# Kernel optimization log

Measured on AMD Instinct MI355X. Metric: run time of the kernel, lower is better.

Reference implementation:

```python
import jax, jax.numpy as jnp
import numpy as np

RESOLUTION = 2 ** 8  # 256
N_POINTS = 2 ** 21


def setup_inputs() -> dict:
    key = jax.random.key(0)
    k1, k2 = jax.random.split(key)
    inp = jax.random.uniform(k1, (N_POINTS, 3), dtype=jnp.float32)
    grid = jax.random.normal(k2, (RESOLUTION, RESOLUTION, RESOLUTION, 3), dtype=jnp.float32) * 0.01
    return {"input": inp, "feature_params": grid}


def reference(input, feature_params):
    R = feature_params.shape[0]
    scaled = input * (R - 1)
    lower = jnp.clip(jnp.floor(scaled).astype(jnp.int32), 0, R - 2)
    upper = jnp.clip(lower + 1, 0, R - 1)
    t = scaled - lower.astype(scaled.dtype)
    xl, yl, zl = lower[:, 0], lower[:, 1], lower[:, 2]
    xu, yu, zu = upper[:, 0], upper[:, 1], upper[:, 2]
    tx, ty, tz = t[:, 0:1], t[:, 1:2], t[:, 2:3]  # (N,1) for broadcast over channels
    # note original indexes grid as [z, y, x]
    c000 = feature_params[zl, yl, xl]
    c001 = feature_params[zl, yl, xu]
    c010 = feature_params[zl, yu, xl]
    c011 = feature_params[zl, yu, xu]
    c100 = feature_params[zu, yl, xl]
    c101 = feature_params[zu, yl, xu]
    c110 = feature_params[zu, yu, xl]
    c111 = feature_params[zu, yu, xu]
    c00 = c000 * (1 - tx) + c001 * tx
    c01 = c010 * (1 - tx) + c011 * tx
    c10 = c100 * (1 - tx) + c101 * tx
    c11 = c110 * (1 - tx) + c111 * tx
    c0 = c00 * (1 - ty) + c01 * ty
    c1 = c10 * (1 - ty) + c11 * ty
    return c0 * (1 - tz) + c1 * tz
```

## Files before the change

### kernel.cpp

```cpp
#include <hip/hip_runtime.h>


#define NB     8192
#define CAP    512u
#define GBLK   1024
#define LAYERF4 1728
#define LAYERF  6912
#define GRIDF4  12582912

#define CUR_OFF   67108864u
#define NEEDED    (67108864u + 32768u)

typedef float f4v __attribute__((ext_vector_type(4)));
typedef float f2v __attribute__((ext_vector_type(2)));
typedef f4v f4u __attribute__((aligned(8)));
typedef f2v f2u __attribute__((aligned(8)));

__device__ __forceinline__ void cell_of(float p, int& l, float& t) {
    float s = p * 255.0f;
    int v = (int)floorf(s);
    v = v < 0 ? 0 : (v > 254 ? 254 : v);
    l = v;
    t = s - (float)v;
}

__device__ __forceinline__ int fine_bin3(float px, float py, float pz) {
    int xl, yl, zl; float tx, ty, tz;
    cell_of(px, xl, tx);
    cell_of(py, yl, ty);
    cell_of(pz, zl, tz);
    return (zl << 5) | (yl >> 3);
}

__device__ __forceinline__ void direct_lerp(const float* __restrict__ grid,
                                            float* __restrict__ out, int i,
                                            int xl, int yl, int zl,
                                            float tx, float ty, float tz) {
    int b00 = (zl * 65536 + yl * 256 + xl) * 3;
    int b01 = b00 + 768, b10 = b00 + 196608, b11 = b10 + 768;
    float s00[6], s01[6], s10[6], s11[6];
#pragma unroll
    for (int k = 0; k < 6; ++k) s00[k] = grid[b00 + k];
#pragma unroll
    for (int k = 0; k < 6; ++k) s01[k] = grid[b01 + k];
#pragma unroll
    for (int k = 0; k < 6; ++k) s10[k] = grid[b10 + k];
#pragma unroll
    for (int k = 0; k < 6; ++k) s11[k] = grid[b11 + k];
#pragma unroll
    for (int c = 0; c < 3; ++c) {
        float c00 = s00[c] * (1.0f - tx) + s00[c + 3] * tx;
        float c01 = s01[c] * (1.0f - tx) + s01[c + 3] * tx;
        float c10 = s10[c] * (1.0f - tx) + s10[c + 3] * tx;
        float c11 = s11[c] * (1.0f - tx) + s11[c + 3] * tx;
        float c0 = c00 * (1.0f - ty) + c01 * ty;
        float c1 = c10 * (1.0f - ty) + c11 * ty;
        out[3 * i + c] = c0 * (1.0f - tz) + c1 * tz;
    }
}

__global__ __launch_bounds__(1024) void k_init(unsigned* __restrict__ cur) {
    int i = blockIdx.x * 1024 + threadIdx.x;
    if (i < NB) cur[i] = (unsigned)i * CAP;
}

__global__ __launch_bounds__(1024) void k_scatter(const float* __restrict__ inp,
                                                  const float* __restrict__ grid,
                                                  float4* __restrict__ binned,
                                                  unsigned* __restrict__ cur,
                                                  float* __restrict__ out, int n) {
    __shared__ unsigned cnt[NB];
    __shared__ unsigned base[NB];
    int t = threadIdx.x;
    int P = n >> 1;
    int stride = gridDim.x * 1024;
    int iters = (P + stride - 1) / stride;

    if ((n & 1) && blockIdx.x == 0 && t == 0) {
        int i = n - 1;
        float px = inp[3 * i], py = inp[3 * i + 1], pz = inp[3 * i + 2];
        int b = fine_bin3(px, py, pz);
        unsigned r = atomicAdd(&cur[b], 1u);
        if (r - (unsigned)b * CAP < CAP) {
            float4 v; v.x = px; v.y = py; v.z = pz; v.w = __uint_as_float((unsigned)i);
            binned[r] = v;
        } else {
            int xl, yl, zl; float tx, ty, tz;
            cell_of(px, xl, tx); cell_of(py, yl, ty); cell_of(pz, zl, tz);
            direct_lerp(grid, out, i, xl, yl, zl, tx, ty, tz);
        }
    }

    for (int it = 0; it < iters; ++it) {
        int pr = it * stride + blockIdx.x * 1024 + t;
        for (int k = t; k < NB; k += 1024) cnt[k] = 0;
        __syncthreads();
        int b0 = 0, b1 = 0; unsigned r0 = 0, r1 = 0;
        float4 p0, p1;
        bool valid = (pr < P);
        if (valid) {
            f4v a = *(const f4u*)(inp + 6 * pr);
            f2v b = *(const f2u*)(inp + 6 * pr + 4);
            p0.x = a.x; p0.y = a.y; p0.z = a.z;
            p0.w = __uint_as_float((unsigned)(2 * pr));
            p1.x = a.w; p1.y = b.x; p1.z = b.y;
            p1.w = __uint_as_float((unsigned)(2 * pr + 1));
            b0 = fine_bin3(p0.x, p0.y, p0.z);
            b1 = fine_bin3(p1.x, p1.y, p1.z);
            r0 = atomicAdd(&cnt[b0], 1u);
            r1 = atomicAdd(&cnt[b1], 1u);
        }
        __syncthreads();
        for (int k = t; k < NB; k += 1024)
            if (cnt[k]) base[k] = atomicAdd(&cur[k], cnt[k]);
        __syncthreads();
        if (valid) {
            unsigned s0 = base[b0] + r0;
            unsigned s1 = base[b1] + r1;
            if (s0 - (unsigned)b0 * CAP < CAP) binned[s0] = p0;
            else {
                int xl, yl, zl; float tx, ty, tz;
                cell_of(p0.x, xl, tx); cell_of(p0.y, yl, ty); cell_of(p0.z, zl, tz);
                direct_lerp(grid, out, 2 * pr, xl, yl, zl, tx, ty, tz);
            }
            if (s1 - (unsigned)b1 * CAP < CAP) binned[s1] = p1;
            else {
                int xl, yl, zl; float tx, ty, tz;
                cell_of(p1.x, xl, tx); cell_of(p1.y, yl, ty); cell_of(p1.z, zl, tz);
                direct_lerp(grid, out, 2 * pr + 1, xl, yl, zl, tx, ty, tz);
            }
        }
        __syncthreads();
    }
}

#define STAGE_LAYER(zg_, slot_)                                                 \
    do {                                                                        \
        size_t basef4 = (size_t)(zg_)*49152 + (size_t)y0 * 192;                 \
        float* dst = &slab[(slot_) * LAYERF];                                   \
        for (int u = t; u < LAYERF4; u += GBLK) {                               \
            size_t sf4 = basef4 + (size_t)u;                                    \
            if (sf4 > (size_t)(GRIDF4 - 1)) sf4 = (size_t)(GRIDF4 - 1);         \
            __builtin_amdgcn_global_load_lds(                                   \
                (const __attribute__((address_space(1))) unsigned int*)(grid + sf4 * 4), \
                (__attribute__((address_space(3))) unsigned int*)&dst[(size_t)u * 4], \
                16, 0, 0);                                                      \
        }                                                                       \
    } while (0)

__global__ __launch_bounds__(GBLK) void k_gather(const float4* __restrict__ binned,
                                                 const float* __restrict__ grid,
                                                 const unsigned* __restrict__ cur,
                                                 float* __restrict__ out) {
    __shared__ __align__(16) float slab[3 * LAYERF];
    int t = threadIdx.x;
    int bin = ((blockIdx.x & 7) << 6) | (blockIdx.x >> 3);
    int zb = bin >> 5;
    int yb = bin & 31;
    int z0 = zb << 4;
    int y0 = yb << 3;

    int zg1 = z0 + 1 > 255 ? 255 : z0 + 1;
    STAGE_LAYER(z0,  0);
    STAGE_LAYER(zg1, 1);

    for (int zc = 0; zc < 16; ++zc) {
        int sA = (zc % 3) * LAYERF;
        int sB = ((zc + 1) % 3) * LAYERF;
        __syncthreads();
        if (zc < 15) {
            int zg = z0 + zc + 2; zg = zg > 255 ? 255 : zg;
            STAGE_LAYER(zg, (zc + 2) % 3);
        }

        int K = ((z0 + zc) << 5) | yb;
        unsigned start = (unsigned)K * CAP;
        unsigned count = cur[K] - start;
        if (count > CAP) count = CAP;

        for (unsigned p = (unsigned)t; p < count; p += (unsigned)GBLK) {
            float4 v = binned[start + p];
            unsigned idx = __float_as_uint(v.w);

            int xl, yl, zl; float tx, ty, tz;
            cell_of(v.x, xl, tx);
            cell_of(v.y, yl, ty);
            cell_of(v.z, zl, tz);
            int row = yl - y0;

            int o00 = sA + row * 768 + xl * 3;
            int o01 = o00 + 768;
            int o10 = sB + row * 768 + xl * 3;
            int o11 = o10 + 768;

#define SEG_READ(b, s)                                   \
            do {                                         \
                int e_ = (b) & ~1;                       \
                bool d_ = ((b) & 1) != 0;                \
                f2v q0 = *(const f2u*)(&slab[e_]);       \
                f2v q1 = *(const f2u*)(&slab[e_ + 2]);   \
                f2v q2 = *(const f2u*)(&slab[e_ + 4]);   \
                f2v q3 = *(const f2u*)(&slab[e_ + 6]);   \
                s[0] = d_ ? q0.y : q0.x;                 \
                s[1] = d_ ? q1.x : q0.y;                 \
                s[2] = d_ ? q1.y : q1.x;                 \
                s[3] = d_ ? q2.x : q1.y;                 \
                s[4] = d_ ? q2.y : q2.x;                 \
                s[5] = d_ ? q3.x : q2.y;                 \
            } while (0)

            float s00[6], s01[6], s10[6], s11[6];
            SEG_READ(o00, s00);
            SEG_READ(o01, s01);
            SEG_READ(o10, s10);
            SEG_READ(o11, s11);
#undef SEG_READ

            float o[3];
#pragma unroll
            for (int c = 0; c < 3; ++c) {
                float c00 = s00[c] * (1.0f - tx) + s00[c + 3] * tx;
                float c01 = s01[c] * (1.0f - tx) + s01[c + 3] * tx;
                float c10 = s10[c] * (1.0f - tx) + s10[c + 3] * tx;
                float c11 = s11[c] * (1.0f - tx) + s11[c + 3] * tx;
                float c0 = c00 * (1.0f - ty) + c01 * ty;
                float c1 = c10 * (1.0f - ty) + c11 * ty;
                o[c] = c0 * (1.0f - tz) + c1 * tz;
            }
            float3 w; w.x = o[0]; w.y = o[1]; w.z = o[2];
            *(float3*)(out + 3 * (size_t)idx) = w;
        }
    }
}

__global__ __launch_bounds__(256) void k_direct(const float* __restrict__ inp,
                                                const float* __restrict__ grid,
                                                float* __restrict__ out, int n) {
    int i = blockIdx.x * blockDim.x + threadIdx.x;
    if (i >= n) return;
    int xl, yl, zl; float tx, ty, tz;
    cell_of(inp[3 * i + 0], xl, tx);
    cell_of(inp[3 * i + 1], yl, ty);
    cell_of(inp[3 * i + 2], zl, tz);
    direct_lerp(grid, out, i, xl, yl, zl, tx, ty, tz);
}

extern "C" void kernel_launch(void* const* d_in, const int* in_sizes, int n_in,
                              void* d_out, int out_size, void* d_ws, size_t ws_size,
                              hipStream_t stream) {
    const float* inp  = (const float*)d_in[0];
    const float* grid = (const float*)d_in[1];
    float* out = (float*)d_out;
    int n = in_sizes[0] / 3;

    if (ws_size < (size_t)NEEDED) {
        int blocks = (n + 255) / 256;
        k_direct<<<blocks, 256, 0, stream>>>(inp, grid, out, n);
        return;
    }

    char* ws = (char*)d_ws;
    float4*   binned = (float4*)ws;
    unsigned* cur    = (unsigned*)(ws + CUR_OFF);

    k_init   <<<8,   1024, 0, stream>>>(cur);
    k_scatter<<<512, 1024, 0, stream>>>(inp, grid, binned, cur, out, n);
    k_gather <<<512, GBLK, 0, stream>>>(binned, grid, cur, out);
}
```

Before: 136.8 us.

## Split gather bins into x-halves with smaller slabs and merged LDS counters

Bins are now split along x into two halves (16384 bins, capacity 256 each), so each gather block stages only half of each z-layer row range (9 rows × 97 float4) into LDS. That gives 1024 smaller 512-thread gather blocks, which should raise occupancy and cut the LDS footprint per block. The scatter kernel reuses a single shared array for both counts and global bases, halving its LDS use. The trade-offs are more global counter atomics, a halo column staged twice at the x split, and lower per-bin capacity, so more points may overflow to the slow direct path.

```diff
diff --git a/kernel.cpp b/kernel.cpp
--- a/kernel.cpp
+++ b/kernel.cpp
@@ -1,15 +1,18 @@
 #include <hip/hip_runtime.h>
 
 
-#define NB     8192
-#define CAP    512u
-#define GBLK   1024
-#define LAYERF4 1728
-#define LAYERF  6912
+#define NB      16384
+#define CAP     256u
+#define SBLK    1024
+#define GBLK    512
+#define CHF4    97
+#define NCH     9
+#define LAYERF4 (NCH * CHF4)
+#define LAYERF  (LAYERF4 * 4)
 #define GRIDF4  12582912
 
 #define CUR_OFF   67108864u
-#define NEEDED    (67108864u + 32768u)
+#define NEEDED    (67108864u + 65536u)
 
 typedef float f4v __attribute__((ext_vector_type(4)));
 typedef float f2v __attribute__((ext_vector_type(2)));
@@ -29,7 +32,7 @@
     cell_of(px, xl, tx);
     cell_of(py, yl, ty);
     cell_of(pz, zl, tz);
-    return (zl << 5) | (yl >> 3);
+    return (zl << 6) | (((yl >> 3) << 1)) | (xl >> 7);
 }
 
 __device__ __forceinline__ void direct_lerp(const float* __restrict__ grid,
@@ -64,16 +67,15 @@
     if (i < NB) cur[i] = (unsigned)i * CAP;
 }
 
-__global__ __launch_bounds__(1024) void k_scatter(const float* __restrict__ inp,
+__global__ __launch_bounds__(SBLK) void k_scatter(const float* __restrict__ inp,
                                                   const float* __restrict__ grid,
                                                   float4* __restrict__ binned,
                                                   unsigned* __restrict__ cur,
                                                   float* __restrict__ out, int n) {
-    __shared__ unsigned cnt[NB];
-    __shared__ unsigned base[NB];
+    __shared__ unsigned agg[NB];
     int t = threadIdx.x;
     int P = n >> 1;
-    int stride = gridDim.x * 1024;
+    int stride = gridDim.x * SBLK;
     int iters = (P + stride - 1) / stride;
 
     if ((n & 1) && blockIdx.x == 0 && t == 0) {
@@ -92,8 +94,8 @@
     }
 
     for (int it = 0; it < iters; ++it) {
-        int pr = it * stride + blockIdx.x * 1024 + t;
-        for (int k = t; k < NB; k += 1024) cnt[k] = 0;
+        int pr = it * stride + blockIdx.x * SBLK + t;
+        for (int k = t; k < NB; k += SBLK) agg[k] = 0;
         __syncthreads();
         int b0 = 0, b1 = 0; unsigned r0 = 0, r1 = 0;
         float4 p0, p1;
@@ -107,16 +109,18 @@
             p1.w = __uint_as_float((unsigned)(2 * pr + 1));
             b0 = fine_bin3(p0.x, p0.y, p0.z);
             b1 = fine_bin3(p1.x, p1.y, p1.z);
-            r0 = atomicAdd(&cnt[b0], 1u);
-            r1 = atomicAdd(&cnt[b1], 1u);
-        }
-        __syncthreads();
-        for (int k = t; k < NB; k += 1024)
-            if (cnt[k]) base[k] = atomicAdd(&cur[k], cnt[k]);
+            r0 = atomicAdd(&agg[b0], 1u);
+            r1 = atomicAdd(&agg[b1], 1u);
+        }
+        __syncthreads();
+        for (int k = t; k < NB; k += SBLK) {
+            unsigned c = agg[k];
+            if (c) agg[k] = atomicAdd(&cur[k], c);
+        }
         __syncthreads();
         if (valid) {
-            unsigned s0 = base[b0] + r0;
-            unsigned s1 = base[b1] + r1;
+            unsigned s0 = agg[b0] + r0;
+            unsigned s1 = agg[b1] + r1;
             if (s0 - (unsigned)b0 * CAP < CAP) binned[s0] = p0;
             else {
                 int xl, yl, zl; float tx, ty, tz;
@@ -136,10 +140,12 @@
 
 #define STAGE_LAYER(zg_, slot_)                                                 \
     do {                                                                        \
-        size_t basef4 = (size_t)(zg_)*49152 + (size_t)y0 * 192;                 \
+        size_t basef4 = (size_t)(zg_)*49152 + (size_t)y0 * 192 + (size_t)xq;    \
         float* dst = &slab[(slot_) * LAYERF];                                   \
         for (int u = t; u < LAYERF4; u += GBLK) {                               \
-            size_t sf4 = basef4 + (size_t)u;                                    \
+            int chunk = u / CHF4;                                               \
+            int j = u - chunk * CHF4;                                           \
+            size_t sf4 = basef4 + (size_t)chunk * 192 + (size_t)j;              \
             if (sf4 > (size_t)(GRIDF4 - 1)) sf4 = (size_t)(GRIDF4 - 1);         \
             __builtin_amdgcn_global_load_lds(                                   \
                 (const __attribute__((address_space(1))) unsigned int*)(grid + sf4 * 4), \
@@ -154,11 +160,14 @@
                                                  float* __restrict__ out) {
     __shared__ __align__(16) float slab[3 * LAYERF];
     int t = threadIdx.x;
-    int bin = ((blockIdx.x & 7) << 6) | (blockIdx.x >> 3);
-    int zb = bin >> 5;
-    int yb = bin & 31;
+    int sb = ((blockIdx.x & 7) << 7) | (blockIdx.x >> 3);
+    int zb = sb >> 6;
+    int yb = (sb >> 1) & 31;
+    int xh = sb & 1;
     int z0 = zb << 4;
     int y0 = yb << 3;
+    int x0 = xh << 7;
+    int xq = xh * 96;
 
     int zg1 = z0 + 1 > 255 ? 255 : z0 + 1;
     STAGE_LAYER(z0,  0);
@@ -173,7 +182,7 @@
             STAGE_LAYER(zg, (zc + 2) % 3);
         }
 
-        int K = ((z0 + zc) << 5) | yb;
+        int K = ((z0 + zc) << 6) | (yb << 1) | xh;
         unsigned start = (unsigned)K * CAP;
         unsigned count = cur[K] - start;
         if (count > CAP) count = CAP;
@@ -187,11 +196,12 @@
             cell_of(v.y, yl, ty);
             cell_of(v.z, zl, tz);
             int row = yl - y0;
-
-            int o00 = sA + row * 768 + xl * 3;
-            int o01 = o00 + 768;
-            int o10 = sB + row * 768 + xl * 3;
-            int o11 = o10 + 768;
+            int xc  = xl - x0;
+
+            int o00 = sA + row * 388 + xc * 3;
+            int o01 = o00 + 388;
+            int o10 = sB + row * 388 + xc * 3;
+            int o11 = o10 + 388;
 
 #define SEG_READ(b, s)                                   \
             do {                                         \
@@ -263,7 +273,7 @@
     float4*   binned = (float4*)ws;
     unsigned* cur    = (unsigned*)(ws + CUR_OFF);
 
-    k_init   <<<8,   1024, 0, stream>>>(cur);
-    k_scatter<<<512, 1024, 0, stream>>>(inp, grid, binned, cur, out, n);
-    k_gather <<<512, GBLK, 0, stream>>>(binned, grid, cur, out);
-}
+    k_init   <<<16,   1024, 0, stream>>>(cur);
+    k_scatter<<<512,  SBLK, 0, stream>>>(inp, grid, binned, cur, out, n);
+    k_gather <<<1024, GBLK, 0, stream>>>(binned, grid, cur, out);
+}
```

Measured after the change: 162.8 us. 1.19x slower.

## Stage grid layers through registers instead of async global-to-LDS loads

Applied to the files above, without the earlier changes.

Replaces the global_load_lds staging of z-layers with explicit register prefetch: the next layer is loaded into registers while the current layer's points are processed, then written to LDS between two barriers. This is meant to avoid the overhead and waitcnt behaviour of direct-to-LDS loads and give the loads more time to complete before they are needed. It adds an extra barrier per layer and raises register pressure in a 1024-thread block.

```diff
diff --git a/kernel.cpp b/kernel.cpp
--- a/kernel.cpp
+++ b/kernel.cpp
@@ -134,18 +134,25 @@
     }
 }
 
-#define STAGE_LAYER(zg_, slot_)                                                 \
-    do {                                                                        \
-        size_t basef4 = (size_t)(zg_)*49152 + (size_t)y0 * 192;                 \
-        float* dst = &slab[(slot_) * LAYERF];                                   \
-        for (int u = t; u < LAYERF4; u += GBLK) {                               \
-            size_t sf4 = basef4 + (size_t)u;                                    \
-            if (sf4 > (size_t)(GRIDF4 - 1)) sf4 = (size_t)(GRIDF4 - 1);         \
-            __builtin_amdgcn_global_load_lds(                                   \
-                (const __attribute__((address_space(1))) unsigned int*)(grid + sf4 * 4), \
-                (__attribute__((address_space(3))) unsigned int*)&dst[(size_t)u * 4], \
-                16, 0, 0);                                                      \
-        }                                                                       \
+#define LOADL(L)                                                        \
+    do {                                                                \
+        int zg = z0 + (L); if (zg > 255) zg = 255;                      \
+        size_t b4 = (size_t)zg * 49152 + (size_t)y0 * 192;              \
+        size_t u0 = b4 + (size_t)t;                                     \
+        if (u0 > (size_t)(GRIDF4 - 1)) u0 = (size_t)(GRIDF4 - 1);       \
+        R0 = *(const f4u*)(grid + u0 * 4);                              \
+        if (t < LAYERF4 - 1024) {                                       \
+            size_t u1 = b4 + 1024 + (size_t)t;                          \
+            if (u1 > (size_t)(GRIDF4 - 1)) u1 = (size_t)(GRIDF4 - 1);   \
+            R1 = *(const f4u*)(grid + u1 * 4);                          \
+        }                                                               \
+    } while (0)
+
+#define WRITEL(slot_)                                                   \
+    do {                                                                \
+        float* dst = &slab[(slot_) * LAYERF];                           \
+        *(f4v*)&dst[(size_t)t * 4] = R0;                                \
+        if (t < LAYERF4 - 1024) *(f4v*)&dst[(size_t)(t + 1024) * 4] = R1; \
     } while (0)
 
 __global__ __launch_bounds__(GBLK) void k_gather(const float4* __restrict__ binned,
@@ -160,18 +167,16 @@
     int z0 = zb << 4;
     int y0 = yb << 3;
 
-    int zg1 = z0 + 1 > 255 ? 255 : z0 + 1;
-    STAGE_LAYER(z0,  0);
-    STAGE_LAYER(zg1, 1);
+    f4v R0, R1;
+
+    LOADL(0); WRITEL(0);
+    LOADL(1); WRITEL(1);
+    LOADL(2);
+    __syncthreads();
 
     for (int zc = 0; zc < 16; ++zc) {
         int sA = (zc % 3) * LAYERF;
         int sB = ((zc + 1) % 3) * LAYERF;
-        __syncthreads();
-        if (zc < 15) {
-            int zg = z0 + zc + 2; zg = zg > 255 ? 255 : zg;
-            STAGE_LAYER(zg, (zc + 2) % 3);
-        }
 
         int K = ((z0 + zc) << 5) | yb;
         unsigned start = (unsigned)K * CAP;
@@ -230,6 +235,11 @@
             float3 w; w.x = o[0]; w.y = o[1]; w.z = o[2];
             *(float3*)(out + 3 * (size_t)idx) = w;
         }
+
+        __syncthreads();
+        if (zc <= 14) WRITEL((zc + 2) % 3);
+        if (zc <= 13) LOADL(zc + 3);
+        __syncthreads();
     }
 }
 
```

After: 133.4 us. 1.03x faster.
